# Optimization experiments

Hardware: AMD Instinct MI355X
Metric: run time of the kernel (lower is better)

The kernel has to match this reference:

```python
import jax, jax.numpy as jnp
import numpy as np

C1 = C2 = COUT = 32
LMAX = 2
N = 8192
FEAT1 = 2 * (1 + 3 + 9) * C1  # 832
WBLK = COUT * C1 * C2


def _enumerate_paths(Lmax):
    paths = []
    for L1 in range(Lmax + 1):
        for L2 in range(Lmax + 1):
            for k in range(min(L1, L2) + 1):
                Lout = L1 + L2 - 2 * k
                if 0 <= Lout <= Lmax:
                    paths.append((L1, L2, Lout, k, False))
            if L1 >= 1 and L2 >= 1:
                for k in range(min(L1 - 1, L2 - 1) + 1):
                    Lout = L1 + L2 - 2 * k - 1
                    if 0 <= Lout <= Lmax:
                        paths.append((L1, L2, Lout, k, True))
    return paths


def _path_eq(L1, L2, k, use_eps):
    # Canonical einsum for one path, fused with the weight mixing 'Zab'
    letters = 'abcdefghijklmnopqrstuvwxyz'
    tl = [c for c in letters if c not in ('a', 'b')]
    i_idx = tl[:L1]
    j_idx = tl[L1:L1 + L2]
    pos = L1 + L2
    for r in range(k):  # pairwise delta contractions on trailing indices
        j_idx[L2 - k + r] = i_idx[L1 - k + r]
    i_free = i_idx[:L1 - k]
    j_free = j_idx[:L2 - k]
    eps_terms = []
    if use_eps:
        ie, je = i_free[-1], j_free[-1]
        i_free, j_free = i_free[:-1], j_free[:-1]
        p = tl[pos]
        eps_terms = [p + ie + je]
        out_idx = i_free + j_free + [p]
    else:
        out_idx = i_free + j_free
    in_terms = ['...a' + ''.join(i_idx), '...b' + ''.join(j_idx)] + eps_terms + ['Zab']
    eq = ','.join(in_terms) + '->...Z' + ''.join(out_idx)
    return eq, len(out_idx)


def _epsilon(dtype):
    e = np.zeros((3, 3, 3), np.float32)
    e[0, 1, 2] = e[1, 2, 0] = e[2, 0, 1] = 1.0
    e[0, 2, 1] = e[2, 1, 0] = e[1, 0, 2] = -1.0
    return jnp.asarray(e, dtype=dtype)


def _split(x, C, Lmax):
    # blocks keyed (s, L): s=0 true tensor, s=1 pseudotensor
    batch = x.shape[:-1]
    out = {}
    idx = 0
    for s in (0, 1):
        for L in range(Lmax + 1):
            d = C * 3 ** L
            blk = x[..., idx:idx + d]
            idx += d
            out[(s, L)] = blk.reshape(*batch, C, *((3,) * L))
    return out


def _forward(x1, x2, weight):
    batch = x1.shape[:-1]
    A = _split(x1, C1, LMAX)
    B = _split(x2, C2, LMAX)
    eps = _epsilon(x1.dtype)
    out = {(s, L): jnp.zeros(batch + (COUT,) + (3,) * L, x1.dtype)
           for s in (0, 1) for L in range(LMAX + 1)}
    w_idx = 0
    for (L1, L2, Lout, k, ue) in _enumerate_paths(LMAX):
        eq, _ = _path_eq(L1, L2, k, ue)
        for s1 in (0, 1):
            for s2 in (0, 1):
                Wp = weight[w_idx:w_idx + WBLK].reshape(COUT, C1, C2)
                w_idx += WBLK
                t1 = A[(s1, L1)]
                t2 = B[(s2, L2)]
                if ue:
                    out_c = jnp.einsum(eq, t1, t2, eps, Wp)
                else:
                    out_c = jnp.einsum(eq, t1, t2, Wp)
                s_out = s1 ^ s2 ^ (1 if ue else 0)
                out[(s_out, Lout)] = out[(s_out, Lout)] + out_c
    parts = [out[(s, L)].reshape(*batch, COUT * 3 ** L)
             for s in (0, 1) for L in range(LMAX + 1)]
    return jnp.concatenate(parts, axis=-1)


def setup_inputs() -> dict:
    key = jax.random.key(0)
    k1, k2, k3 = jax.random.split(key, 3)
    n_paths = len(_enumerate_paths(LMAX))  # 15
    wn = n_paths * 4 * WBLK  # 1966080
    x1 = jax.random.normal(k1, (N, FEAT1), dtype=jnp.float32)
    x2 = jax.random.normal(k2, (N, FEAT1), dtype=jnp.float32)
    weight = jax.random.normal(k3, (wn,), dtype=jnp.float32) * 0.02
    return {"x1": x1, "x2": x2, "weight": weight}


def reference(x1, x2, weight):
    return _forward(x1, x2, weight)
```

## Files before the change

### kernel.cpp

```cpp
#include <hip/hip_runtime.h>

#define DEVINL __device__ __forceinline__

typedef unsigned int  uint32;
typedef unsigned short u16;

typedef short bf16x8  __attribute__((ext_vector_type(8)));
typedef float f32x16  __attribute__((ext_vector_type(16)));
typedef float fx2     __attribute__((ext_vector_type(2)));

union U4H { uint4 u; bf16x8 h; };

constexpr int PL1c[15] = {0,0,0,1,1,1,1,1,1,2,2,2,2,2,2};
constexpr int PL2c[15] = {0,1,2,0,1,1,1,2,2,0,1,1,2,2,2};
constexpr int PLOc[15] = {0,1,2,1,2,0,1,1,2,2,1,2,2,0,1};
constexpr int PTc [15] = {1,1,1,1,1,3,2,3,2,1,3,2,3,9,6};
constexpr int PW3c[3]  = {1,3,9};
constexpr int LOFFc[3] = {0,32,128};

constexpr int GCNT[6] = {6,6,12,12,12,12};
constexpr int GNT [6] = {1,1,3,3,9,9};
__device__ const int g_combo[6][12][3] = {
  {{0,0,0},{0,1,1},{5,0,0},{5,1,1},{13,0,0},{13,1,1},
   {0,0,0},{0,0,0},{0,0,0},{0,0,0},{0,0,0},{0,0,0}},
  {{0,0,1},{0,1,0},{5,0,1},{5,1,0},{13,0,1},{13,1,0},
   {0,0,0},{0,0,0},{0,0,0},{0,0,0},{0,0,0},{0,0,0}},
  {{1,0,0},{1,1,1},{3,0,0},{3,1,1},{7,0,0},{7,1,1},{10,0,0},{10,1,1},
   {6,0,1},{6,1,0},{14,0,1},{14,1,0}},
  {{1,0,1},{1,1,0},{3,0,1},{3,1,0},{7,0,1},{7,1,0},{10,0,1},{10,1,0},
   {6,0,0},{6,1,1},{14,0,0},{14,1,1}},
  {{2,0,0},{2,1,1},{4,0,0},{4,1,1},{9,0,0},{9,1,1},{12,0,0},{12,1,1},
   {8,0,1},{8,1,0},{11,0,1},{11,1,0}},
  {{2,0,1},{2,1,0},{4,0,1},{4,1,0},{9,0,1},{9,1,0},{12,0,1},{12,1,0},
   {8,0,0},{8,1,1},{11,0,0},{11,1,1}},
};

struct Terms { int iA[9]; int jB[9]; int sg[9]; };

DEVINL Terms make_terms(int path, int mo) {
  Terms t{};
  switch (path) {
    case 0:  t.iA[0]=0;  t.jB[0]=0;  t.sg[0]=1; break;
    case 1:  t.iA[0]=0;  t.jB[0]=mo; t.sg[0]=1; break;
    case 2:  t.iA[0]=0;  t.jB[0]=mo; t.sg[0]=1; break;
    case 3:  t.iA[0]=mo; t.jB[0]=0;  t.sg[0]=1; break;
    case 4:  t.iA[0]=mo/3; t.jB[0]=mo%3; t.sg[0]=1; break;
    case 5:  for (int v=0;v<3;++v){t.iA[v]=v; t.jB[v]=v; t.sg[v]=1;} break;
    case 6:  {int p=mo,u1=(p+1)%3,u2=(p+2)%3;
              t.iA[0]=u1; t.jB[0]=u2; t.sg[0]= 1;
              t.iA[1]=u2; t.jB[1]=u1; t.sg[1]=-1;} break;
    case 7:  {int x=mo; for(int u=0;u<3;++u){t.iA[u]=u; t.jB[u]=3*x+u; t.sg[u]=1;}} break;
    case 8:  {int x=mo/3,p=mo%3,u1=(p+1)%3,u2=(p+2)%3;
              t.iA[0]=u1; t.jB[0]=3*x+u2; t.sg[0]= 1;
              t.iA[1]=u2; t.jB[1]=3*x+u1; t.sg[1]=-1;} break;
    case 9:  t.iA[0]=mo; t.jB[0]=0; t.sg[0]=1; break;
    case 10: {int u=mo; for(int v=0;v<3;++v){t.iA[v]=3*u+v; t.jB[v]=v; t.sg[v]=1;}} break;
    case 11: {int u=mo/3,p=mo%3,v1=(p+1)%3,v2=(p+2)%3;
              t.iA[0]=3*u+v1; t.jB[0]=v2; t.sg[0]= 1;
              t.iA[1]=3*u+v2; t.jB[1]=v1; t.sg[1]=-1;} break;
    case 12: {int u=mo/3,x=mo%3; for(int v=0;v<3;++v){t.iA[v]=3*u+v; t.jB[v]=3*x+v; t.sg[v]=1;}} break;
    case 13: for (int w=0;w<9;++w){t.iA[w]=w; t.jB[w]=w; t.sg[w]=1;} break;
    case 14: {int p=mo,u1=(p+1)%3,u2=(p+2)%3;
              for(int v=0;v<3;++v){
                t.iA[2*v]  =3*u1+v; t.jB[2*v]  =3*u2+v; t.sg[2*v]  = 1;
                t.iA[2*v+1]=3*u2+v; t.jB[2*v+1]=3*u1+v; t.sg[2*v+1]=-1;}} break;
  }
  return t;
}

DEVINL u16 f2bf(float f) {
  uint32 u = __float_as_uint(f);
  u += 0x7fffu + ((u >> 16) & 1u);
  return (u16)(u >> 16);
}
DEVINL float bf2f(u16 h) { return __uint_as_float(((uint32)h) << 16); }

DEVINL void unpack8(uint4 r, fx2 out[4]) {
  uint32 c[4] = {r.x, r.y, r.z, r.w};
#pragma unroll
  for (int q = 0; q < 4; ++q) {
    out[q].x = __uint_as_float(c[q] << 16);
    out[q].y = __uint_as_float(c[q] & 0xffff0000u);
  }
}

DEVINL bf16x8 packA(const fx2 p[4]) {
  U4H r;
  r.u.x = __builtin_amdgcn_perm(__float_as_uint(p[0].y), __float_as_uint(p[0].x), 0x07060302u);
  r.u.y = __builtin_amdgcn_perm(__float_as_uint(p[1].y), __float_as_uint(p[1].x), 0x07060302u);
  r.u.z = __builtin_amdgcn_perm(__float_as_uint(p[2].y), __float_as_uint(p[2].x), 0x07060302u);
  r.u.w = __builtin_amdgcn_perm(__float_as_uint(p[3].y), __float_as_uint(p[3].x), 0x07060302u);
  return r.h;
}

DEVINL f32x16 mfma32(bf16x8 a, uint4 w, f32x16 c) {
  U4H x; x.u = w;
  return __builtin_amdgcn_mfma_f32_32x32x16_bf16(a, x.h, c, 0, 0, 0);
}

template<int PATH, int NTC, int MOB>
DEVINL void run_combo(int s1, int s2, int n0,
                      const u16* __restrict__ x2t, const u16* x1l,
                      const uint4* wlds, f32x16* acc, int lane, int wv)
{
  constexpr int L1v = PL1c[PATH];
  constexpr int L2v = PL2c[PATH];
  constexpr int T   = PTc[PATH];
  constexpr int P1v = PW3c[L1v];
  constexpr int NCH = (T + 2) / 3;
  const int bh   = wv & 1;
  const int a0   = (wv >> 1) * 8;
  const int nloc = lane & 31;
  const int oct  = lane >> 5;
  const u16* bb = x2t + (size_t)(n0 + nloc) * 832 + s2 * 416 + LOFFc[L2v]
                + bh * 16 + oct * 8;
  const u16* ab = x1l + nloc * 836 + s1 * 416 + LOFFc[L1v];
  const uint4* wbase = wlds + ((a0 * 2 + bh) << 6) + lane;
#pragma unroll
  for (int m = 0; m < NTC; ++m) {
    const Terms tm = make_terms(PATH, MOB + m);
#pragma unroll
    for (int tc = 0; tc < NCH; ++tc) {
      constexpr int TLO0 = 0;  (void)TLO0;
      const int tlo = tc * 3;
      const int tn  = (T - tlo < 3) ? (T - tlo) : 3;
      fx2 b2[3][4];
#pragma unroll
      for (int u = 0; u < 3; ++u)
        if (u < tn) {
          uint4 rv = *(const uint4*)(bb + tm.jB[tlo + u] * 32);
          unpack8(rv, b2[u]);
        }
#pragma unroll
      for (int ia = 0; ia < 8; ++ia) {
        fx2 p[4];
#pragma unroll
        for (int u = 0; u < 3; ++u) {
          if (u < tn) {
            float av = bf2f(ab[(a0 + ia) * P1v + tm.iA[tlo + u]]);
            if (tm.sg[tlo + u] < 0) av = -av;
            fx2 a2; a2.x = av; a2.y = av;
            if (u == 0) {
#pragma unroll
              for (int q = 0; q < 4; ++q) p[q] = a2 * b2[0][q];
            } else {
#pragma unroll
              for (int q = 0; q < 4; ++q)
                p[q] = __builtin_elementwise_fma(a2, b2[u][q], p[q]);
            }
          }
        }
        uint4 wfr = wbase[ia * 128];
        acc[m] = mfma32(packA(p), wfr, acc[m]);
      }
    }
  }
}

template<int G, int MOB, int NTC>
DEVINL void process_chunk(int n0, const u16* __restrict__ x2t, const u16* x1l,
                          uint4* wlds, const uint4* __restrict__ Wb,
                          float* red, int tid, int lane, int wv)
{
  constexpr int lout = G >> 1;
  f32x16 acc[NTC];
#pragma unroll
  for (int t = 0; t < NTC; ++t)
#pragma unroll
    for (int e = 0; e < 16; ++e) acc[t][e] = 0.f;

#pragma unroll 1
  for (int ci = 0; ci < GCNT[G]; ++ci) {
    const int path = g_combo[G][ci][0];
    const int s1   = g_combo[G][ci][1];
    const int s2   = g_combo[G][ci][2];
    const int pc   = path * 4 + s1 * 2 + s2;
    __syncthreads();
    {
      const uint4* srcw = Wb + ((size_t)pc << 12);
#pragma unroll
      for (int it = 0; it < 8; ++it) {
        int idx = tid + it * 512;
        __builtin_amdgcn_global_load_lds(
            (const __attribute__((address_space(1))) unsigned int*)(srcw + idx),
            (__attribute__((address_space(3))) unsigned int*)(&wlds[idx]),
            16, 0, 0);
      }
    }
    __syncthreads();
#define RCASE(P) case P: if constexpr (PLOc[P] == lout) \
      run_combo<P, NTC, MOB>(s1, s2, n0, x2t, x1l, wlds, acc, lane, wv); break;
    switch (path) {
      RCASE(0) RCASE(1) RCASE(2) RCASE(3) RCASE(4) RCASE(5) RCASE(6) RCASE(7)
      RCASE(8) RCASE(9) RCASE(10) RCASE(11) RCASE(12) RCASE(13) RCASE(14)
    }
#undef RCASE
    __builtin_amdgcn_sched_barrier(0);
  }
  const int col = lane & 31, oct = lane >> 5;
#pragma unroll
  for (int t = 0; t < NTC; ++t)
#pragma unroll
    for (int r = 0; r < 16; ++r) {
      int row = (r & 3) + 8 * (r >> 2) + 4 * oct;
      atomicAdd(&red[(((MOB + t) * 32 + row) << 5) + col], acc[t][r]);
    }
}

template<int G>
DEVINL void process_group(int n0, const u16* __restrict__ x2t, const u16* x1l,
                          uint4* wlds, const uint4* __restrict__ Wb, float* red,
                          float* __restrict__ out, int tid, int lane, int wv)
{
  constexpr int NTF   = GNT[G];
  constexpr int s_out = G & 1;
  constexpr int lout  = G >> 1;
  __syncthreads();
  for (int i = tid; i < 1024 * NTF; i += 512) red[i] = 0.f;
  __syncthreads();
  if constexpr (NTF == 9) {
    process_chunk<G, 0, 3>(n0, x2t, x1l, wlds, Wb, red, tid, lane, wv);
    process_chunk<G, 3, 3>(n0, x2t, x1l, wlds, Wb, red, tid, lane, wv);
    process_chunk<G, 6, 3>(n0, x2t, x1l, wlds, Wb, red, tid, lane, wv);
  } else {
    process_chunk<G, 0, NTF>(n0, x2t, x1l, wlds, Wb, red, tid, lane, wv);
  }
  __syncthreads();
  constexpr int obase = s_out * 416 + LOFFc[lout];
  constexpr int span  = 32 * NTF;
  for (int o = tid; o < 32 * span; o += 512) {
    int row = o / span; int c = o - row * span;
    int Z = c / NTF;    int mo = c - Z * NTF;
    out[(size_t)(n0 + row) * 832 + obase + c] = red[((mo * 32 + row) << 5) + Z];
  }
}

__global__ __launch_bounds__(512, 2)
void k_main(const float* __restrict__ x1, const u16* __restrict__ x2t,
            const uint4* __restrict__ Wb, float* __restrict__ out)
{
  __shared__ u16   x1l[32 * 836];
  __shared__ uint4 wlds[4096];
  __shared__ float red[9216];
  const int tid  = threadIdx.x;
  const int lane = tid & 63, wv = tid >> 6;
  const int n0   = blockIdx.x * 32;

  {
    int rr = tid >> 4, c0 = tid & 15;
    const float* src = x1 + (size_t)(n0 + rr) * 832;
#pragma unroll 4
    for (int jj = 0; jj < 52; ++jj) {
      int colx = c0 + jj * 16;
      x1l[rr * 836 + colx] = f2bf(src[colx]);
    }
  }

  process_group<0>(n0, x2t, x1l, wlds, Wb, red, out, tid, lane, wv);
  process_group<1>(n0, x2t, x1l, wlds, Wb, red, out, tid, lane, wv);
  process_group<2>(n0, x2t, x1l, wlds, Wb, red, out, tid, lane, wv);
  process_group<3>(n0, x2t, x1l, wlds, Wb, red, out, tid, lane, wv);
  process_group<4>(n0, x2t, x1l, wlds, Wb, red, out, tid, lane, wv);
  process_group<5>(n0, x2t, x1l, wlds, Wb, red, out, tid, lane, wv);
}

__global__ void k_convw(const float* __restrict__ w, u16* __restrict__ Wb) {
  int o  = blockIdx.x * 1024 + threadIdx.x;
  int j  = o & 7;
  int l  = (o >> 3) & 63;
  int bh = (o >> 9) & 1;
  int a  = (o >> 10) & 31;
  int pc = o >> 15;
  int Z  = l & 31;
  int b  = bh * 16 + ((l >> 5) & 1) * 8 + j;
  float f = w[((size_t)pc << 15) + (size_t)Z * 1024 + a * 32 + b];
  Wb[o] = f2bf(f);
}

__global__ void k_convx2(const float* __restrict__ x2, u16* __restrict__ x2t) {
  int o = blockIdx.x * 1024 + threadIdx.x;
  int n = o / 832; int r = o - n * 832;
  int s = (r >= 416); int r2 = r - s * 416;
  int L = (r2 >= 32) + (r2 >= 128);
  int off = (L == 0) ? 0 : ((L == 1) ? 32 : 128);
  int c = r2 - off;
  int j = c >> 5, b = c & 31;
  int p3 = (L == 0) ? 1 : ((L == 1) ? 3 : 9);
  float f = x2[(size_t)n * 832 + s * 416 + off + b * p3 + j];
  x2t[o] = f2bf(f);
}

extern "C" void kernel_launch(void* const* d_in, const int* in_sizes, int n_in,
                              void* d_out, int out_size, void* d_ws, size_t ws_size,
                              hipStream_t stream) {
  const float* x1 = (const float*)d_in[0];
  const float* x2 = (const float*)d_in[1];
  const float* w  = (const float*)d_in[2];
  float* out = (float*)d_out;
  u16* Wb  = (u16*)d_ws;
  u16* x2t = (u16*)((char*)d_ws + (4u << 20));
  (void)in_sizes; (void)n_in; (void)out_size; (void)ws_size;

  k_convw <<<1920, 1024, 0, stream>>>(w, Wb);
  k_convx2<<<6656, 1024, 0, stream>>>(x2, x2t);
  k_main  <<<256, 512, 0, stream>>>(x1, x2t, (const uint4*)Wb, out);
}
```

Measured before the change: 826.4 us.

## Split output groups across two blocks per tile and read weights directly from global

Each 32-row tile is now handled by two blocks, each computing three of the six output groups, balanced by the number of output components. This doubles the grid. The LDS weight staging and its two barriers per combo are removed, so MFMA weight fragments are read straight from global/L2. The reduction buffer shrinks to one chunk with a per-chunk writeback, which cuts LDS use so launch bounds can allow more blocks per CU. In exchange, x1 conversion is duplicated per block and weight reads now depend on cache hit rates.

```diff
diff --git a/kernel.cpp b/kernel.cpp
--- a/kernel.cpp
+++ b/kernel.cpp
@@ -101,7 +101,8 @@
 template<int PATH, int NTC, int MOB>
 DEVINL void run_combo(int s1, int s2, int n0,
                       const u16* __restrict__ x2t, const u16* x1l,
-                      const uint4* wlds, f32x16* acc, int lane, int wv)
+                      const uint4* __restrict__ wgl,
+                      f32x16* acc, int lane, int wv)
 {
   constexpr int L1v = PL1c[PATH];
   constexpr int L2v = PL2c[PATH];
@@ -115,13 +116,12 @@
   const u16* bb = x2t + (size_t)(n0 + nloc) * 832 + s2 * 416 + LOFFc[L2v]
                 + bh * 16 + oct * 8;
   const u16* ab = x1l + nloc * 836 + s1 * 416 + LOFFc[L1v];
-  const uint4* wbase = wlds + ((a0 * 2 + bh) << 6) + lane;
+  const uint4* wbase = wgl + ((a0 * 2 + bh) << 6) + lane;
 #pragma unroll
   for (int m = 0; m < NTC; ++m) {
     const Terms tm = make_terms(PATH, MOB + m);
 #pragma unroll
     for (int tc = 0; tc < NCH; ++tc) {
-      constexpr int TLO0 = 0;  (void)TLO0;
       const int tlo = tc * 3;
       const int tn  = (T - tlo < 3) ? (T - tlo) : 3;
       fx2 b2[3][4];
@@ -159,15 +159,20 @@
 
 template<int G, int MOB, int NTC>
 DEVINL void process_chunk(int n0, const u16* __restrict__ x2t, const u16* x1l,
-                          uint4* wlds, const uint4* __restrict__ Wb,
-                          float* red, int tid, int lane, int wv)
+                          const uint4* __restrict__ Wb, float* red,
+                          float* __restrict__ out, int tid, int lane, int wv)
 {
-  constexpr int lout = G >> 1;
+  constexpr int lout  = G >> 1;
+  constexpr int s_out = G & 1;
+  constexpr int NTF   = GNT[G];
+  __syncthreads();
+  for (int i = tid; i < 1024 * NTC; i += 512) red[i] = 0.f;
   f32x16 acc[NTC];
 #pragma unroll
   for (int t = 0; t < NTC; ++t)
 #pragma unroll
     for (int e = 0; e < 16; ++e) acc[t][e] = 0.f;
+  __syncthreads();
 
 #pragma unroll 1
   for (int ci = 0; ci < GCNT[G]; ++ci) {
@@ -175,21 +180,9 @@
     const int s1   = g_combo[G][ci][1];
     const int s2   = g_combo[G][ci][2];
     const int pc   = path * 4 + s1 * 2 + s2;
-    __syncthreads();
-    {
-      const uint4* srcw = Wb + ((size_t)pc << 12);
-#pragma unroll
-      for (int it = 0; it < 8; ++it) {
-        int idx = tid + it * 512;
-        __builtin_amdgcn_global_load_lds(
-            (const __attribute__((address_space(1))) unsigned int*)(srcw + idx),
-            (__attribute__((address_space(3))) unsigned int*)(&wlds[idx]),
-            16, 0, 0);
-      }
-    }
-    __syncthreads();
+    const uint4* wgl = Wb + ((size_t)pc << 12);
 #define RCASE(P) case P: if constexpr (PLOc[P] == lout) \
-      run_combo<P, NTC, MOB>(s1, s2, n0, x2t, x1l, wlds, acc, lane, wv); break;
+      run_combo<P, NTC, MOB>(s1, s2, n0, x2t, x1l, wgl, acc, lane, wv); break;
     switch (path) {
       RCASE(0) RCASE(1) RCASE(2) RCASE(3) RCASE(4) RCASE(5) RCASE(6) RCASE(7)
       RCASE(8) RCASE(9) RCASE(10) RCASE(11) RCASE(12) RCASE(13) RCASE(14)
@@ -203,48 +196,45 @@
 #pragma unroll
     for (int r = 0; r < 16; ++r) {
       int row = (r & 3) + 8 * (r >> 2) + 4 * oct;
-      atomicAdd(&red[(((MOB + t) * 32 + row) << 5) + col], acc[t][r]);
+      atomicAdd(&red[((t * 32 + row) << 5) + col], acc[t][r]);
     }
+  __syncthreads();
+  constexpr int obase = s_out * 416 + LOFFc[lout];
+  for (int o = tid; o < 1024 * NTC; o += 512) {
+    int t   = o % NTC;
+    int zr  = o / NTC;
+    int Z   = zr & 31;
+    int row = zr >> 5;
+    out[(size_t)(n0 + row) * 832 + obase + Z * NTF + (MOB + t)]
+        = red[((t * 32 + row) << 5) + Z];
+  }
 }
 
 template<int G>
 DEVINL void process_group(int n0, const u16* __restrict__ x2t, const u16* x1l,
-                          uint4* wlds, const uint4* __restrict__ Wb, float* red,
+                          const uint4* __restrict__ Wb, float* red,
                           float* __restrict__ out, int tid, int lane, int wv)
 {
-  constexpr int NTF   = GNT[G];
-  constexpr int s_out = G & 1;
-  constexpr int lout  = G >> 1;
-  __syncthreads();
-  for (int i = tid; i < 1024 * NTF; i += 512) red[i] = 0.f;
-  __syncthreads();
-  if constexpr (NTF == 9) {
-    process_chunk<G, 0, 3>(n0, x2t, x1l, wlds, Wb, red, tid, lane, wv);
-    process_chunk<G, 3, 3>(n0, x2t, x1l, wlds, Wb, red, tid, lane, wv);
-    process_chunk<G, 6, 3>(n0, x2t, x1l, wlds, Wb, red, tid, lane, wv);
+  if constexpr (GNT[G] == 9) {
+    process_chunk<G, 0, 3>(n0, x2t, x1l, Wb, red, out, tid, lane, wv);
+    process_chunk<G, 3, 3>(n0, x2t, x1l, Wb, red, out, tid, lane, wv);
+    process_chunk<G, 6, 3>(n0, x2t, x1l, Wb, red, out, tid, lane, wv);
   } else {
-    process_chunk<G, 0, NTF>(n0, x2t, x1l, wlds, Wb, red, tid, lane, wv);
-  }
-  __syncthreads();
-  constexpr int obase = s_out * 416 + LOFFc[lout];
-  constexpr int span  = 32 * NTF;
-  for (int o = tid; o < 32 * span; o += 512) {
-    int row = o / span; int c = o - row * span;
-    int Z = c / NTF;    int mo = c - Z * NTF;
-    out[(size_t)(n0 + row) * 832 + obase + c] = red[((mo * 32 + row) << 5) + Z];
-  }
-}
-
-__global__ __launch_bounds__(512, 2)
+    process_chunk<G, 0, GNT[G]>(n0, x2t, x1l, Wb, red, out, tid, lane, wv);
+  }
+}
+
+__global__ __launch_bounds__(512, 4)
 void k_main(const float* __restrict__ x1, const u16* __restrict__ x2t,
             const uint4* __restrict__ Wb, float* __restrict__ out)
 {
   __shared__ u16   x1l[32 * 836];
-  __shared__ uint4 wlds[4096];
-  __shared__ float red[9216];
+  __shared__ float red[3072];
   const int tid  = threadIdx.x;
   const int lane = tid & 63, wv = tid >> 6;
-  const int n0   = blockIdx.x * 32;
+  const int tile = blockIdx.x >> 1;
+  const int part = blockIdx.x & 1;
+  const int n0   = tile * 32;
 
   {
     int rr = tid >> 4, c0 = tid & 15;
@@ -256,12 +246,15 @@
     }
   }
 
-  process_group<0>(n0, x2t, x1l, wlds, Wb, red, out, tid, lane, wv);
-  process_group<1>(n0, x2t, x1l, wlds, Wb, red, out, tid, lane, wv);
-  process_group<2>(n0, x2t, x1l, wlds, Wb, red, out, tid, lane, wv);
-  process_group<3>(n0, x2t, x1l, wlds, Wb, red, out, tid, lane, wv);
-  process_group<4>(n0, x2t, x1l, wlds, Wb, red, out, tid, lane, wv);
-  process_group<5>(n0, x2t, x1l, wlds, Wb, red, out, tid, lane, wv);
+  if (part == 0) {
+    process_group<4>(n0, x2t, x1l, Wb, red, out, tid, lane, wv);
+    process_group<2>(n0, x2t, x1l, Wb, red, out, tid, lane, wv);
+    process_group<1>(n0, x2t, x1l, Wb, red, out, tid, lane, wv);
+  } else {
+    process_group<5>(n0, x2t, x1l, Wb, red, out, tid, lane, wv);
+    process_group<3>(n0, x2t, x1l, Wb, red, out, tid, lane, wv);
+    process_group<0>(n0, x2t, x1l, Wb, red, out, tid, lane, wv);
+  }
 }
 
 __global__ void k_convw(const float* __restrict__ w, u16* __restrict__ Wb) {
@@ -303,5 +296,5 @@
 
   k_convw <<<1920, 1024, 0, stream>>>(w, Wb);
   k_convx2<<<6656, 1024, 0, stream>>>(x2, x2t);
-  k_main  <<<256, 512, 0, stream>>>(x1, x2t, (const uint4*)Wb, out);
-}
+  k_main  <<<512, 512, 0, stream>>>(x1, x2t, (const uint4*)Wb, out);
+}
```

Result: slower. 1.699 ms (+105.6%).
